# Performance work log

Hardware: AMD Instinct MI355X
Metric: run time of the kernel (lower is better)

## Reference

```python
import jax, jax.numpy as jnp
import numpy as np

L, B, T, D, V = 2, 16, 20, 768, 30000


def setup_inputs() -> dict:
    key = jax.random.key(0)
    k1, k2, k3, k4 = jax.random.split(key, 4)
    answer_embed = jax.random.normal(k1, (L, B, T, D), dtype=jnp.float32)
    vocab_embed = 0.1 * jax.random.normal(k2, (V, D), dtype=jnp.float32)
    # classifier_transform modeled as Linear(D, D): y = x @ W.T + b
    W = jax.random.normal(k3, (D, D), dtype=jnp.float32) * (1.0 / np.sqrt(D))
    b = jax.random.normal(k4, (D,), dtype=jnp.float32) * 0.01
    return {"answer_embed": answer_embed, "vocab_embed": vocab_embed, "W": W, "b": b}


def reference(answer_embed, vocab_embed, W, b):
    # vocab_classifiers: [V, D] after the linear transform
    vocab_classifiers = vocab_embed @ W.T + b
    # Original: broadcast multiply [L,B,T,D,1]*[1,1,1,D,V] then sum over D.
    # Mathematically identical contraction over D -> [L, B, T, V]
    return jnp.einsum('lbtd,vd->lbtv', answer_embed, vocab_classifiers)
```

## Files before the change

kernel.cpp:

```cpp
#include <hip/hip_runtime.h>

#define KDIM 768
#define MANS 640
#define VV   30000
#define NGRP 235
#define VELEM (VV * KDIM)
#define CVTBLK ((VELEM + 8191) / 8192)
#define A2BLK  ((MANS / 64) * (KDIM / 128))

typedef __attribute__((ext_vector_type(4)))  float  f32x4;
typedef __attribute__((ext_vector_type(16))) float  f32x16;
typedef __attribute__((ext_vector_type(8)))  __bf16 bf16x8;
typedef __attribute__((ext_vector_type(8)))  unsigned short ushort8;

__device__ __forceinline__ unsigned short f2bf(float f) {
    union { __bf16 h; unsigned short u; } t;
    t.h = (__bf16)f;
    return t.u;
}

__device__ __forceinline__ ushort8 cvt8(f32x4 a, f32x4 b) {
    union { bf16x8 h; ushort8 u; } c;
    c.h[0] = (__bf16)a.x; c.h[1] = (__bf16)a.y;
    c.h[2] = (__bf16)a.z; c.h[3] = (__bf16)a.w;
    c.h[4] = (__bf16)b.x; c.h[5] = (__bf16)b.y;
    c.h[6] = (__bf16)b.z; c.h[7] = (__bf16)b.w;
    return c.u;
}

__device__ __forceinline__ void load_lds16(const unsigned short* g, unsigned short* l) {
    __builtin_amdgcn_global_load_lds(
        (__attribute__((address_space(1))) void*)(void*)g,
        (__attribute__((address_space(3))) void*)l,
        16, 0, 0);
}

__global__ __launch_bounds__(256) void prep_small(
    const float* __restrict__ W, const float* __restrict__ A,
    const float* __restrict__ b, unsigned short* __restrict__ Wt_bf,
    float* __restrict__ cvec)
{
    __shared__ float ts[64][65];
    const int blk = blockIdx.x;
    if (blk < 144) {
        int bx = (blk % 12) * 64, by = (blk / 12) * 64;
        int tx = threadIdx.x & 63, tg = threadIdx.x >> 6;
#pragma unroll
        for (int i = 0; i < 16; ++i) {
            int r = tg * 16 + i;
            ts[r][tx] = W[(long)(by + r) * KDIM + bx + tx];
        }
        __syncthreads();
#pragma unroll
        for (int i = 0; i < 16; ++i) {
            int r = tg * 16 + i;
            Wt_bf[(long)(bx + r) * KDIM + by + tx] = f2bf(ts[tx][r]);
        }
    } else {
        int row  = (blk - 144) * 4 + (threadIdx.x >> 6);
        int lane = threadIdx.x & 63;
        const float* ap = A + (long)row * KDIM;
        float s = 0.f;
#pragma unroll
        for (int i = 0; i < KDIM / 64; ++i) s += ap[i * 64 + lane] * b[i * 64 + lane];
#pragma unroll
        for (int off = 32; off; off >>= 1) s += __shfl_down(s, off, 64);
        if (lane == 0) cvec[row] = s;
    }
}

__global__ __launch_bounds__(256) void gemm_a2(
    const float* __restrict__ Af, const unsigned short* __restrict__ Bp,
    unsigned short* __restrict__ outp,
    const float* __restrict__ vocab, unsigned short* __restrict__ vocab_bf)
{
    if (blockIdx.x >= A2BLK) {
        const long base = (long)(blockIdx.x - A2BLK) * 8192 + (long)threadIdx.x * 8;
#pragma unroll
        for (int p = 0; p < 4; ++p) {
            long idx = base + p * 2048;
            if (idx < VELEM) {
                f32x4 v0 = ((const f32x4*)(vocab + idx))[0];
                f32x4 v1 = ((const f32x4*)(vocab + idx))[1];
                *(ushort8*)(vocab_bf + idx) = cvt8(v0, v1);
            }
        }
        return;
    }

    constexpr int TM = 64, TN = 128;
    __shared__ unsigned short sA[TM * 64];
    __shared__ unsigned short sB[TN * 64];

    const int t    = threadIdx.x;
    const int lane = t & 63;
    const int w    = t >> 6;
    const int wm   = w >> 1;
    const int wn   = w & 1;
    const int half = lane >> 5;
    const int col  = lane & 31;
    const long m0  = (long)(blockIdx.x % (MANS / 64)) * TM;
    const long n0  = (long)(blockIdx.x / (MANS / 64)) * TN;

    f32x16 acc[2];
    acc[0] = (f32x16)(0.f);
    acc[1] = (f32x16)(0.f);

    const float* gaf[2]; int laOff[2];
#pragma unroll
    for (int j = 0; j < 2; ++j) {
        int s   = (j * 4 + w) * 64 + lane;
        int row = s >> 3;
        int c   = (s & 7) ^ (row & 7);
        gaf[j]   = Af + (m0 + row) * KDIM + c * 8;
        laOff[j] = s * 8;
    }
    const unsigned short* gb[4]; unsigned short* lbB[4];
#pragma unroll
    for (int j = 0; j < 4; ++j) {
        int s   = (j * 4 + w) * 64 + lane;
        int row = s >> 3;
        int c   = (s & 7) ^ (row & 7);
        gb[j]  = Bp + (n0 + row) * KDIM + c * 8;
        lbB[j] = &sB[(j * 4 + w) * 64 * 8];
    }

    for (int k0 = 0; k0 < KDIM; k0 += 64) {
#pragma unroll
        for (int j = 0; j < 4; ++j) load_lds16(gb[j] + k0, lbB[j]);
#pragma unroll
        for (int j = 0; j < 2; ++j) {
            f32x4 v0 = ((const f32x4*)(gaf[j] + k0))[0];
            f32x4 v1 = ((const f32x4*)(gaf[j] + k0))[1];
            *(ushort8*)(&sA[0] + laOff[j]) = cvt8(v0, v1);
        }
        __syncthreads();

#pragma unroll
        for (int g = 0; g < 4; ++g) {
            const int cg = g * 2 + half;
            int arow = wm * 32 + col;
            bf16x8 af = *(const bf16x8*)&sA[(arow * 8 + (cg ^ (arow & 7))) * 8];
#pragma unroll
            for (int fn = 0; fn < 2; ++fn) {
                int brow = wn * 64 + fn * 32 + col;
                bf16x8 bfv = *(const bf16x8*)&sB[(brow * 8 + (cg ^ (brow & 7))) * 8];
                acc[fn] = __builtin_amdgcn_mfma_f32_32x32x16_bf16(
                    af, bfv, acc[fn], 0, 0, 0);
            }
        }
        __syncthreads();
    }

#pragma unroll
    for (int fn = 0; fn < 2; ++fn) {
        long n = n0 + wn * 64 + fn * 32 + col;
#pragma unroll
        for (int rg = 0; rg < 16; ++rg) {
            long m = m0 + wm * 32 + (rg & 3) + 8 * (rg >> 2) + 4 * half;
            outp[m * KDIM + n] = f2bf(acc[fn][rg]);
        }
    }
}

__global__ __launch_bounds__(256) void gemm_big(
    const unsigned short* __restrict__ A, const unsigned short* __restrict__ Bbf,
    const float* __restrict__ cvec, float* __restrict__ outp)
{
    const int id    = blockIdx.x;
    const int x     = id & 7;
    const int q     = id >> 3;
    const int m_idx = q % 5;
    const int n_grp = (q / 5) * 8 + x;
    if (n_grp >= NGRP) return;

    __shared__ unsigned short sA[128 * 64];
    __shared__ unsigned short sB[128 * 64];

    const int t    = threadIdx.x;
    const int lane = t & 63;
    const int w    = t >> 6;
    const int wm   = w >> 1;
    const int wn   = w & 1;
    const int half = lane >> 5;
    const int col  = lane & 31;
    const long m0  = (long)m_idx * 128;
    const long n0  = (long)n_grp * 128;

    f32x16 acc[2][2];
#pragma unroll
    for (int i = 0; i < 2; ++i)
#pragma unroll
        for (int j = 0; j < 2; ++j) acc[i][j] = (f32x16)(0.f);

    const unsigned short* ga[4];
    unsigned short*       laA[4];
#pragma unroll
    for (int j = 0; j < 4; ++j) {
        int s   = (j * 4 + w) * 64 + lane;
        int row = s >> 3;
        int c   = (s & 7) ^ (row & 7);
        ga[j]  = A + (m0 + row) * KDIM + c * 8;
        laA[j] = &sA[(j * 4 + w) * 64 * 8];
    }
    const unsigned short* gb[4];
    unsigned short*       laB[4];
#pragma unroll
    for (int j = 0; j < 4; ++j) {
        int s   = (j * 4 + w) * 64 + lane;
        int row = s >> 3;
        int c   = (s & 7) ^ (row & 7);
        long grow = n0 + row;
        if (grow > VV - 1) grow = VV - 1;
        gb[j]  = Bbf + grow * KDIM + c * 8;
        laB[j] = &sB[(j * 4 + w) * 64 * 8];
    }

    for (int k0 = 0; k0 < KDIM; k0 += 64) {
#pragma unroll
        for (int j = 0; j < 4; ++j) load_lds16(ga[j] + k0, laA[j]);
#pragma unroll
        for (int j = 0; j < 4; ++j) load_lds16(gb[j] + k0, laB[j]);
        __syncthreads();

#pragma unroll
        for (int g = 0; g < 4; ++g) {
            const int cg = g * 2 + half;
            bf16x8 af[2], bfr[2];
#pragma unroll
            for (int fm = 0; fm < 2; ++fm) {
                int row = wm * 64 + fm * 32 + col;
                af[fm] = *(const bf16x8*)&sA[(row * 8 + (cg ^ (row & 7))) * 8];
            }
#pragma unroll
            for (int fn = 0; fn < 2; ++fn) {
                int row = wn * 64 + fn * 32 + col;
                bfr[fn] = *(const bf16x8*)&sB[(row * 8 + (cg ^ (row & 7))) * 8];
            }
#pragma unroll
            for (int fm = 0; fm < 2; ++fm)
#pragma unroll
                for (int fn = 0; fn < 2; ++fn)
                    acc[fm][fn] = __builtin_amdgcn_mfma_f32_32x32x16_bf16(
                        af[fm], bfr[fn], acc[fm][fn], 0, 0, 0);
        }
        __syncthreads();
    }

#pragma unroll
    for (int fm = 0; fm < 2; ++fm)
#pragma unroll
        for (int fn = 0; fn < 2; ++fn) {
            long n = n0 + wn * 64 + fn * 32 + col;
            if (n < VV) {
#pragma unroll
                for (int rg = 0; rg < 16; ++rg) {
                    long m = m0 + wm * 64 + fm * 32
                           + (rg & 3) + 8 * (rg >> 2) + 4 * half;
                    outp[m * (long)VV + n] = acc[fm][fn][rg] + cvec[m];
                }
            }
        }
}

extern "C" void kernel_launch(void* const* d_in, const int* in_sizes, int n_in,
                              void* d_out, int out_size, void* d_ws, size_t ws_size,
                              hipStream_t stream) {
    const float* answer = (const float*)d_in[0];
    const float* vocab  = (const float*)d_in[1];
    const float* W      = (const float*)d_in[2];
    const float* bvec   = (const float*)d_in[3];

    char* ws = (char*)d_ws;
    unsigned short* Wt_bf   = (unsigned short*)ws;
    unsigned short* A2_bf   = (unsigned short*)(ws + 1179648);
    float*          cptr    = (float*)(ws + 1179648 + 983040);
    unsigned short* vocabbf = (unsigned short*)(ws + 2165248);

    prep_small<<<304, 256, 0, stream>>>(W, answer, bvec, Wt_bf, cptr);

    gemm_a2<<<A2BLK + CVTBLK, 256, 0, stream>>>(answer, Wt_bf, A2_bf, vocab, vocabbf);

    gemm_big<<<1200, 256, 0, stream>>>(A2_bf, vocabbf, cptr, (float*)d_out);
}
```

Measured before the change: 222.2 us.

## Pre-swizzle A into MFMA fragment layout and double-buffer B tiles in LDS

```diff
diff --git a/kernel.cpp b/kernel.cpp
--- a/kernel.cpp
+++ b/kernel.cpp
@@ -4,6 +4,7 @@
 #define MANS 640
 #define VV   30000
 #define NGRP 235
+#define NKS  (KDIM / 64)
 #define VELEM (VV * KDIM)
 #define CVTBLK ((VELEM + 8191) / 8192)
 #define A2BLK  ((MANS / 64) * (KDIM / 128))
@@ -33,6 +34,13 @@
         (__attribute__((address_space(1))) void*)(void*)g,
         (__attribute__((address_space(3))) void*)l,
         16, 0, 0);
+}
+
+__device__ __forceinline__ long a2f_off(int m, int n) {
+    int mb = m >> 7, wm = (m >> 6) & 1, fm = (m >> 5) & 1, colm = m & 31;
+    int kt = n >> 6, g = (n >> 4) & 3, halfb = (n >> 3) & 1, e = n & 7;
+    return ((((long)(mb * 12 + kt) * 2 + wm) * 2 + fm) * 4 + g) * 512
+         + (halfb * 32 + colm) * 8 + e;
 }
 
 __global__ __launch_bounds__(256) void prep_small(
@@ -154,11 +162,11 @@
 
 #pragma unroll
     for (int fn = 0; fn < 2; ++fn) {
-        long n = n0 + wn * 64 + fn * 32 + col;
+        int n = (int)n0 + wn * 64 + fn * 32 + col;
 #pragma unroll
         for (int rg = 0; rg < 16; ++rg) {
-            long m = m0 + wm * 32 + (rg & 3) + 8 * (rg >> 2) + 4 * half;
-            outp[m * KDIM + n] = f2bf(acc[fn][rg]);
+            int m = (int)m0 + wm * 32 + (rg & 3) + 8 * (rg >> 2) + 4 * half;
+            outp[a2f_off(m, n)] = f2bf(acc[fn][rg]);
         }
     }
 }
@@ -174,8 +182,7 @@
     const int n_grp = (q / 5) * 8 + x;
     if (n_grp >= NGRP) return;
 
-    __shared__ unsigned short sA[128 * 64];
-    __shared__ unsigned short sB[128 * 64];
+    __shared__ unsigned short sB[2][128 * 64];
 
     const int t    = threadIdx.x;
     const int lane = t & 63;
@@ -184,7 +191,6 @@
     const int wn   = w & 1;
     const int half = lane >> 5;
     const int col  = lane & 31;
-    const long m0  = (long)m_idx * 128;
     const long n0  = (long)n_grp * 128;
 
     f32x16 acc[2][2];
@@ -193,18 +199,11 @@
 #pragma unroll
         for (int j = 0; j < 2; ++j) acc[i][j] = (f32x16)(0.f);
 
-    const unsigned short* ga[4];
-    unsigned short*       laA[4];
-#pragma unroll
-    for (int j = 0; j < 4; ++j) {
-        int s   = (j * 4 + w) * 64 + lane;
-        int row = s >> 3;
-        int c   = (s & 7) ^ (row & 7);
-        ga[j]  = A + (m0 + row) * KDIM + c * 8;
-        laA[j] = &sA[(j * 4 + w) * 64 * 8];
-    }
+    const unsigned short* aBase = A + (((long)(m_idx * 12) * 2 + wm) * 2) * 4 * 512
+                                    + lane * 8;
+
     const unsigned short* gb[4];
-    unsigned short*       laB[4];
+    int lbOff[4];
 #pragma unroll
     for (int j = 0; j < 4; ++j) {
         int s   = (j * 4 + w) * 64 + lane;
@@ -212,30 +211,31 @@
         int c   = (s & 7) ^ (row & 7);
         long grow = n0 + row;
         if (grow > VV - 1) grow = VV - 1;
-        gb[j]  = Bbf + grow * KDIM + c * 8;
-        laB[j] = &sB[(j * 4 + w) * 64 * 8];
-    }
-
-    for (int k0 = 0; k0 < KDIM; k0 += 64) {
-#pragma unroll
-        for (int j = 0; j < 4; ++j) load_lds16(ga[j] + k0, laA[j]);
-#pragma unroll
-        for (int j = 0; j < 4; ++j) load_lds16(gb[j] + k0, laB[j]);
-        __syncthreads();
-
+        gb[j]    = Bbf + grow * KDIM + c * 8;
+        lbOff[j] = (j * 4 + w) * 64 * 8;
+    }
+
+    auto stage = [&](int kt, int buf) {
+        const int o = buf * (128 * 64);
+#pragma unroll
+        for (int j = 0; j < 4; ++j)
+            load_lds16(gb[j] + kt * 64, &sB[0][0] + o + lbOff[j]);
+    };
+
+    auto compute = [&](int kt, int buf) {
+        const unsigned short* bB = &sB[0][0] + buf * (128 * 64);
+        const unsigned short* aK = aBase + (long)kt * 8192;
 #pragma unroll
         for (int g = 0; g < 4; ++g) {
             const int cg = g * 2 + half;
             bf16x8 af[2], bfr[2];
 #pragma unroll
-            for (int fm = 0; fm < 2; ++fm) {
-                int row = wm * 64 + fm * 32 + col;
-                af[fm] = *(const bf16x8*)&sA[(row * 8 + (cg ^ (row & 7))) * 8];
-            }
+            for (int fm = 0; fm < 2; ++fm)
+                af[fm] = *(const bf16x8*)(aK + fm * 2048 + g * 512);
 #pragma unroll
             for (int fn = 0; fn < 2; ++fn) {
                 int row = wn * 64 + fn * 32 + col;
-                bfr[fn] = *(const bf16x8*)&sB[(row * 8 + (cg ^ (row & 7))) * 8];
+                bfr[fn] = *(const bf16x8*)&bB[(row * 8 + (cg ^ (row & 7))) * 8];
             }
 #pragma unroll
             for (int fm = 0; fm < 2; ++fm)
@@ -244,9 +244,23 @@
                     acc[fm][fn] = __builtin_amdgcn_mfma_f32_32x32x16_bf16(
                         af[fm], bfr[fn], acc[fm][fn], 0, 0, 0);
         }
-        __syncthreads();
-    }
-
+    };
+
+    stage(0, 0);
+    asm volatile("s_waitcnt vmcnt(0)" ::: "memory");
+    __builtin_amdgcn_s_barrier();
+
+    int p = 0;
+    for (int kt = 0; kt < NKS - 1; ++kt) {
+        stage(kt + 1, p ^ 1);
+        compute(kt, p);
+        asm volatile("s_waitcnt vmcnt(0)" ::: "memory");
+        __builtin_amdgcn_s_barrier();
+        p ^= 1;
+    }
+    compute(NKS - 1, p);
+
+    const long m0 = (long)m_idx * 128;
 #pragma unroll
     for (int fm = 0; fm < 2; ++fm)
 #pragma unroll
@@ -273,13 +287,13 @@
 
     char* ws = (char*)d_ws;
     unsigned short* Wt_bf   = (unsigned short*)ws;
-    unsigned short* A2_bf   = (unsigned short*)(ws + 1179648);
+    unsigned short* A2F     = (unsigned short*)(ws + 1179648);
     float*          cptr    = (float*)(ws + 1179648 + 983040);
     unsigned short* vocabbf = (unsigned short*)(ws + 2165248);
 
     prep_small<<<304, 256, 0, stream>>>(W, answer, bvec, Wt_bf, cptr);
 
-    gemm_a2<<<A2BLK + CVTBLK, 256, 0, stream>>>(answer, Wt_bf, A2_bf, vocab, vocabbf);
-
-    gemm_big<<<1200, 256, 0, stream>>>(A2_bf, vocabbf, cptr, (float*)d_out);
-}
+    gemm_a2<<<A2BLK + CVTBLK, 256, 0, stream>>>(answer, Wt_bf, A2F, vocab, vocabbf);
+
+    gemm_big<<<1200, 256, 0, stream>>>(A2F, vocabbf, cptr, (float*)d_out);
+}
```

Measured after the change: 222.0 us. About the same (-0.1%).
